# Optimization experiments

Hardware: AMD Instinct MI355X
Metric: run time of the kernel (lower is better)

The kernel has to match this reference:

```python
import jax, jax.numpy as jnp
import numpy as np
from jax import lax

B, C_IN, H, W = 16, 2048, 16, 16
HIDDEN, N_ANC = 512, 9
N_POS, N_NEG = 2048, 2048
TOT = B * N_ANC * H * W  # 36864 = flat conf logits; also rows of reg.view(-1,4)


def _xyxy_to_cxcywh(b):
    x1, y1, x2, y2 = b[..., 0], b[..., 1], b[..., 2], b[..., 3]
    return jnp.stack([(x1 + x2) * 0.5, (y1 + y2) * 0.5, x2 - x1, y2 - y1], axis=-1)


def _cxcywh_to_xyxy(b):
    cx, cy, w, h = b[..., 0], b[..., 1], b[..., 2], b[..., 3]
    return jnp.stack([cx - w * 0.5, cy - h * 0.5, cx + w * 0.5, cy + h * 0.5], axis=-1)


def _rand_boxes(key, n):
    # valid xyxy boxes on the 16x16 feature-map coordinate grid, w,h in [1,4]
    k1, k2 = jax.random.split(key)
    xy = jax.random.uniform(k1, (n, 2), jnp.float32) * 12.0
    wh = 1.0 + jax.random.uniform(k2, (n, 2), jnp.float32) * 3.0
    return jnp.concatenate([xy, xy + wh], axis=-1)


def setup_inputs() -> dict:
    key = jax.random.key(0)
    ks = jax.random.split(key, 10)
    feature_map = jax.random.normal(ks[0], (B, C_IN, H, W), jnp.float32)
    pos_anc_ind = jax.random.randint(ks[1], (N_POS,), 0, TOT)
    neg_anc_ind = jax.random.randint(ks[2], (N_NEG,), 0, TOT)
    pos_anc_coords = _rand_boxes(ks[3], N_POS)
    gt_bboxes_pos = _rand_boxes(ks[4], N_POS)
    s1 = 1.0 / np.sqrt(C_IN * 9)
    W1 = jax.random.uniform(ks[5], (HIDDEN, C_IN, 3, 3), jnp.float32, -s1, s1)
    b1 = jnp.zeros((HIDDEN,), jnp.float32)
    s2 = 1.0 / np.sqrt(HIDDEN)
    Wc = jax.random.uniform(ks[6], (N_ANC, HIDDEN), jnp.float32, -s2, s2)
    bc = jnp.zeros((N_ANC,), jnp.float32)
    Wr = jax.random.uniform(ks[7], (N_ANC * 4, HIDDEN), jnp.float32, -s2, s2)
    br = jnp.zeros((N_ANC * 4,), jnp.float32)
    return {"feature_map": feature_map, "pos_anc_coords": pos_anc_coords,
            "gt_bboxes_pos": gt_bboxes_pos, "W1": W1, "b1": b1, "Wc": Wc,
            "bc": bc, "Wr": Wr, "br": br,
            "pos_anc_ind": pos_anc_ind, "neg_anc_ind": neg_anc_ind}


def generate_proposals(anchors, offsets):
    a = _xyxy_to_cxcywh(anchors)
    p = jnp.stack([a[:, 0] + offsets[:, 0] * a[:, 2],
                   a[:, 1] + offsets[:, 1] * a[:, 3],
                   a[:, 2] * jnp.exp(offsets[:, 2]),
                   a[:, 3] * jnp.exp(offsets[:, 3])], axis=-1)
    return _cxcywh_to_xyxy(p)


def calc_gt_offsets(anc, gt):
    a = _xyxy_to_cxcywh(anc)
    g = _xyxy_to_cxcywh(gt)
    tx = (g[:, 0] - a[:, 0]) / a[:, 2]
    ty = (g[:, 1] - a[:, 1]) / a[:, 3]
    tw = jnp.log(g[:, 2] / a[:, 2])
    th = jnp.log(g[:, 3] / a[:, 3])
    return jnp.stack([tx, ty, tw, th], axis=-1)


def reference(feature_map, pos_anc_coords, gt_bboxes_pos, W1, b1, Wc, bc, Wr, br,
              pos_anc_ind, neg_anc_ind):
    # ProposalModule: conv3x3 -> (dropout=identity in eval) -> relu -> 1x1 heads
    out = lax.conv_general_dilated(feature_map, W1, (1, 1), 'SAME',
                                   dimension_numbers=('NCHW', 'OIHW', 'NCHW'))
    out = jax.nn.relu(out + b1[None, :, None, None])
    conf = jnp.einsum('bchw,oc->bohw', out, Wc) + bc[None, :, None, None]   # [B,9,H,W]
    reg = jnp.einsum('bchw,oc->bohw', out, Wr) + br[None, :, None, None]    # [B,36,H,W]
    # irregular flat gathers, exactly mirroring torch .flatten()/.view(-1,4)
    conf_pos = conf.reshape(-1)[pos_anc_ind]
    conf_neg = conf.reshape(-1)[neg_anc_ind]
    offsets_pos = reg.reshape(-1, 4)[pos_anc_ind]
    proposals = generate_proposals(pos_anc_coords, offsets_pos)
    gt_offsets = calc_gt_offsets(pos_anc_coords, gt_bboxes_pos)
    # BCE-with-logits, targets 1 for pos / 0 for neg, reduction='sum' / B
    cls_loss = (jnp.sum(jax.nn.softplus(-conf_pos)) + jnp.sum(jax.nn.softplus(conf_neg))) / B
    # smooth L1 (beta=1), reduction='sum' / B
    d = offsets_pos - gt_offsets
    ad = jnp.abs(d)
    reg_loss = jnp.sum(jnp.where(ad < 1.0, 0.5 * d * d, ad - 0.5)) / B
    total_rpn_loss = 1.0 * cls_loss + 5.0 * reg_loss  # w_conf=1, w_reg=5
    return total_rpn_loss, proposals
```

## Files before the change

kernel.cpp:

```cpp
#include <hip/hip_runtime.h>
#include <hip/hip_bf16.h>
#include <stdint.h>

#define CIN 2048
#define HID 512
#define NPOS 2048
#define NNEG 2048

#define BM 256
#define BN 256
#define BK 64
#define NS 8
#define A_ELEMS (BM * BK)
#define B_ELEMS (BN * BK)

typedef __attribute__((ext_vector_type(8))) short s16x8;
typedef __attribute__((ext_vector_type(4))) short s16x4;
typedef __attribute__((ext_vector_type(4))) float f32x4;
typedef unsigned short ushort_t;

static __device__ __forceinline__ float bf2f(unsigned short u) {
    union { float f; unsigned int i; } v; v.i = ((unsigned int)u) << 16; return v.f;
}
static __device__ __forceinline__ unsigned short f2bf(float f) {
    union { float f; unsigned int i; } v; v.f = f;
    unsigned int r = v.i + 0x7FFF + ((v.i >> 16) & 1);
    return (unsigned short)(r >> 16);
}

typedef __attribute__((address_space(1))) const void gvoid_t;
typedef __attribute__((address_space(3))) void lvoid_t;
static __device__ __forceinline__ void gload16(const void* g, void* l) {
    __builtin_amdgcn_global_load_lds((gvoid_t*)g, (lvoid_t*)l, 16, 0, 0);
}

__global__ __launch_bounds__(256) void k_prep(const float* __restrict__ F,
                                              const float* __restrict__ W1,
                                              ushort_t* __restrict__ Fp,
                                              ushort_t* __restrict__ Wt2) {
    __shared__ float tile[64][17];
    __shared__ float buf[512 * 9];
    int bid = blockIdx.x;
    int t = threadIdx.x;
    if (bid < 1024) {
        int b = bid >> 6, rem = bid & 63;
        int y = rem >> 2, icq = rem & 3;
        for (int i = 0; i < 8; ++i) {
            int ic0 = icq * 512 + i * 64;
            {
                int ci = t >> 2, xg = t & 3;
                const float4 v = *(const float4*)&F[((size_t)(b * CIN + ic0 + ci) * 16 + y) * 16 + xg * 4];
                tile[ci][xg * 4 + 0] = v.x;
                tile[ci][xg * 4 + 1] = v.y;
                tile[ci][xg * 4 + 2] = v.z;
                tile[ci][xg * 4 + 3] = v.w;
            }
            __syncthreads();
            {
                int x = t >> 4, cig = t & 15;
                s16x4 o;
#pragma unroll
                for (int j = 0; j < 4; ++j) o[j] = (short)f2bf(tile[cig * 4 + j][x]);
                *(s16x4*)&Fp[((size_t)(b * 18 + y + 1) * 18 + (x + 1)) * CIN + ic0 + cig * 4] = o;
            }
            __syncthreads();
        }
    } else if (bid < 1536) {
        int oc = bid - 1024;
        for (int ic0 = 0; ic0 < CIN; ic0 += 512) {
            const float* src = W1 + ((size_t)oc * CIN + ic0) * 9;
            {
                const float4* s4 = (const float4*)src;
                float4* b4 = (float4*)buf;
                for (int i = t; i < 1152; i += 256) b4[i] = s4[i];
            }
            __syncthreads();
            for (int s = t; s < 9 * 64; s += 256) {
                int k = s >> 6, g = s & 63;
                s16x8 v;
#pragma unroll
                for (int j = 0; j < 8; ++j) v[j] = (short)f2bf(buf[(g * 8 + j) * 9 + k]);
                *(s16x8*)&Wt2[((size_t)(k * HID + oc)) * CIN + ic0 + g * 8] = v;
            }
            __syncthreads();
        }
    } else {
        const s16x8 z = {0, 0, 0, 0, 0, 0, 0, 0};
        for (int idx = (bid - 1536) * 256 + t; idx < 16 * 68 * 256; idx += 64 * 256) {
            int seg = idx & 255;
            int cell = (idx >> 8) % 68;
            int b = idx / (68 * 256);
            int Y, X;
            if (cell < 18)      { Y = 0;         X = cell; }
            else if (cell < 36) { Y = 17;        X = cell - 18; }
            else if (cell < 52) { Y = cell - 35; X = 0; }
            else                { Y = cell - 51; X = 17; }
            *(s16x8*)&Fp[((size_t)(b * 18 + Y) * 18 + X) * CIN + seg * 8] = z;
        }
    }
}

__global__ __launch_bounds__(512, 2) void k_gemm(const ushort_t* __restrict__ Fp,
                                                 const ushort_t* __restrict__ Wt2,
                                                 ushort_t* __restrict__ Part,
                                                 int icLen, int nPairs) {
    extern __shared__ ushort_t ldsbuf[];
    ushort_t* As = ldsbuf;
    ushort_t* Bs = ldsbuf + 2 * A_ELEMS;

    int bid = blockIdx.x;
    int rb = bid / nPairs;
    int pair = bid - rb * nPairs;
    int split = pair >> 1, cb = pair & 1;
    int icBase = split * icLen;
    int m0 = rb * BM, oc0 = cb * BN;
    int t = threadIdx.x;
    int wid = t >> 6, lane = t & 63;
    int wr = wid >> 2, wn = wid & 3;
    int hi = lane >> 4, lo = lane & 15;

    f32x4 acc[8][4];
#pragma unroll
    for (int a = 0; a < 8; ++a)
#pragma unroll
        for (int b = 0; b < 4; ++b) acc[a][b] = (f32x4){0.f, 0.f, 0.f, 0.f};

    int Abase[4], Bbase[4];
#pragma unroll
    for (int j = 0; j < 4; ++j) {
        int li = j * 512 + t;
        int row = li >> 3;
        int sg = (li & 7) ^ (row & 7);
        int m = m0 + row;
        int b = m >> 8, y = (m >> 4) & 15, x = m & 15;
        Abase[j] = ((b * 18 + y) * 18 + x) * CIN + sg * 8;
        Bbase[j] = (oc0 + row) * CIN + sg * 8;
    }
    int aidx[8][2], bidx[4][2];
#pragma unroll
    for (int fm = 0; fm < 8; ++fm)
#pragma unroll
        for (int ks = 0; ks < 2; ++ks) {
            int r = wr * 128 + fm * 16 + lo;
            aidx[fm][ks] = r * BK + ((ks * 32 + hi * 8) ^ ((r & 7) << 3));
        }
#pragma unroll
    for (int fn = 0; fn < 4; ++fn)
#pragma unroll
        for (int ks = 0; ks < 2; ++ks) {
            int rB = wn * 64 + fn * 16 + lo;
            bidx[fn][ks] = rB * BK + ((ks * 32 + hi * 8) ^ ((rB & 7) << 3));
        }

    const int nsteps = (icLen / BK) * 9;

#define STAGE(BUF, S)                                                                \
    do {                                                                             \
        int kidx_ = (S) % 9, icc_ = (S) / 9;                                         \
        int ak_ = ((kidx_ / 3) * 18 + (kidx_ - 3 * (kidx_ / 3))) * CIN + icBase + icc_ * BK; \
        int bk_ = kidx_ * HID * CIN + icBase + icc_ * BK;                            \
        ushort_t* dA_ = As + (BUF) * A_ELEMS;                                        \
        ushort_t* dB_ = Bs + (BUF) * B_ELEMS;                                        \
        _Pragma("unroll") for (int j_ = 0; j_ < 4; ++j_) {                           \
            gload16(Fp + Abase[j_] + ak_, dA_ + (size_t)(j_ * 512 + t) * 8);         \
            gload16(Wt2 + Bbase[j_] + bk_, dB_ + (size_t)(j_ * 512 + t) * 8);        \
        }                                                                            \
    } while (0)

    STAGE(0, 0);
    asm volatile("s_waitcnt vmcnt(0)" ::: "memory");
    __builtin_amdgcn_s_barrier();
    __builtin_amdgcn_sched_barrier(0);

    int cur = 0;
#pragma unroll 1
    for (int step = 0; step < nsteps; ++step) {
        const ushort_t* cA = As + cur * A_ELEMS;
        const ushort_t* cB = Bs + cur * B_ELEMS;
        if (step + 1 < nsteps) STAGE(cur ^ 1, step + 1);
        s16x8 af[8][2], bf[4][2];
#pragma unroll
        for (int ks = 0; ks < 2; ++ks) {
#pragma unroll
            for (int fm = 0; fm < 8; ++fm) af[fm][ks] = *(const s16x8*)&cA[aidx[fm][ks]];
#pragma unroll
            for (int fn = 0; fn < 4; ++fn) bf[fn][ks] = *(const s16x8*)&cB[bidx[fn][ks]];
        }
        __builtin_amdgcn_s_setprio(1);
#pragma unroll
        for (int fm = 0; fm < 8; ++fm)
#pragma unroll
            for (int fn = 0; fn < 4; ++fn)
#pragma unroll
                for (int ks = 0; ks < 2; ++ks)
                    acc[fm][fn] = __builtin_amdgcn_mfma_f32_16x16x32_bf16(
                        af[fm][ks], bf[fn][ks], acc[fm][fn], 0, 0, 0);
        __builtin_amdgcn_s_setprio(0);
        if (step + 1 < nsteps) {
            asm volatile("s_waitcnt vmcnt(0)" ::: "memory");
            __builtin_amdgcn_s_barrier();
            __builtin_amdgcn_sched_barrier(0);
        }
        cur ^= 1;
    }
#undef STAGE

#pragma unroll
    for (int fm = 0; fm < 8; ++fm)
#pragma unroll
        for (int fn = 0; fn < 4; ++fn)
#pragma unroll
            for (int r = 0; r < 4; ++r) {
                int gm = m0 + wr * 128 + fm * 16 + hi * 4 + r;
                int gn = oc0 + wn * 64 + fn * 16 + lo;
                Part[((size_t)split * 4096 + gm) * HID + gn] = f2bf(acc[fm][fn][r]);
            }
}

__global__ __launch_bounds__(256) void k_heads(const ushort_t* __restrict__ Part, int ns,
                                               const float* __restrict__ b1,
                                               const float* __restrict__ Wc,
                                               const float* __restrict__ bc,
                                               const float* __restrict__ Wr,
                                               const float* __restrict__ br,
                                               float* __restrict__ conf,
                                               float* __restrict__ reg) {
    extern __shared__ ushort_t hsm[];
    ushort_t* Ah = hsm;
    ushort_t* Wh = hsm + 16 * HID;
    int t = threadIdx.x;
    int wid = t >> 6, lane = t & 63;
    int hi = lane >> 4, lo = lane & 15;
    int row0 = blockIdx.x * 16;

#pragma unroll
    for (int i = 0; i < 4; ++i) {
        int pos = i * 256 + t;
        int r = pos >> 6, sg = pos & 63;
        float s[8];
#pragma unroll
        for (int j = 0; j < 8; ++j) s[j] = 0.f;
        for (int sp = 0; sp < ns; ++sp) {
            s16x8 v = *(const s16x8*)&Part[((size_t)sp * 4096 + row0 + r) * HID + sg * 8];
#pragma unroll
            for (int j = 0; j < 8; ++j) s[j] += bf2f((unsigned short)v[j]);
        }
        s16x8 o;
#pragma unroll
        for (int j = 0; j < 8; ++j) o[j] = (short)f2bf(fmaxf(s[j] + b1[sg * 8 + j], 0.f));
        *(s16x8*)&Ah[r * HID + ((sg ^ (r & 7)) << 3)] = o;
    }
#pragma unroll
    for (int i = 0; i < 12; ++i) {
        int sid = i * 256 + t;
        int o = sid >> 6, sg = sid & 63;
        s16x8 v;
#pragma unroll
        for (int j = 0; j < 8; ++j) {
            float w = 0.f;
            if (o < 9) w = Wc[o * HID + sg * 8 + j];
            else if (o < 45) w = Wr[(size_t)(o - 9) * HID + sg * 8 + j];
            v[j] = (short)f2bf(w);
        }
        *(s16x8*)&Wh[o * HID + ((sg ^ (o & 7)) << 3)] = v;
    }
    __syncthreads();
    if (wid != 0) return;

    f32x4 acc[3];
#pragma unroll
    for (int fn = 0; fn < 3; ++fn) acc[fn] = (f32x4){0.f, 0.f, 0.f, 0.f};
#pragma unroll 1
    for (int kf = 0; kf < 16; ++kf) {
        int rA = lo;
        s16x8 a_ = *(const s16x8*)&Ah[rA * HID + ((kf * 32 + hi * 8) ^ ((rA & 7) << 3))];
#pragma unroll
        for (int fn = 0; fn < 3; ++fn) {
            int rB = fn * 16 + lo;
            s16x8 b_ = *(const s16x8*)&Wh[rB * HID + ((kf * 32 + hi * 8) ^ ((rB & 7) << 3))];
            acc[fn] = __builtin_amdgcn_mfma_f32_16x16x32_bf16(a_, b_, acc[fn], 0, 0, 0);
        }
    }
#pragma unroll
    for (int fn = 0; fn < 3; ++fn)
#pragma unroll
        for (int r = 0; r < 4; ++r) {
            int gm = row0 + hi * 4 + r;
            int o = fn * 16 + lo;
            float v = acc[fn][r];
            if (o < 9) conf[gm * 9 + o] = v + bc[o];
            else if (o < 45) reg[gm * 36 + (o - 9)] = v + br[o - 9];
        }
}

static __device__ __forceinline__ float softplus(float x) {
    return log1pf(expf(-fabsf(x))) + fmaxf(x, 0.f);
}

__global__ __launch_bounds__(1024) void k_loss(const float* __restrict__ conf,
                                               const float* __restrict__ reg,
                                               const int* __restrict__ pos_ind,
                                               const int* __restrict__ neg_ind,
                                               const float* __restrict__ anc,
                                               const float* __restrict__ gt,
                                               float* __restrict__ out) {
    int t = threadIdx.x;
    float cls = 0.f, rloss = 0.f;
    for (int p = t; p < NPOS; p += 1024) {
        int ind = pos_ind[p];
        {
            int b = ind / 2304, r = ind % 2304;
            int c = r >> 8, r2 = r & 255;
            float cv = conf[(b * 256 + r2) * 9 + c];
            cls += softplus(-cv);
        }
        float off[4];
#pragma unroll
        for (int j = 0; j < 4; ++j) {
            int e = 4 * ind + j;
            int b = e / 9216, r = e % 9216;
            int c = r >> 8, r2 = r & 255;
            off[j] = reg[(b * 256 + r2) * 36 + c];
        }
        float ax1 = anc[4 * p], ay1 = anc[4 * p + 1], ax2 = anc[4 * p + 2], ay2 = anc[4 * p + 3];
        float acx = (ax1 + ax2) * 0.5f, acy = (ay1 + ay2) * 0.5f;
        float aw = ax2 - ax1, ah = ay2 - ay1;
        float pcx = acx + off[0] * aw, pcy = acy + off[1] * ah;
        float pw = aw * expf(off[2]), ph = ah * expf(off[3]);
        out[1 + 4 * p + 0] = pcx - pw * 0.5f;
        out[1 + 4 * p + 1] = pcy - ph * 0.5f;
        out[1 + 4 * p + 2] = pcx + pw * 0.5f;
        out[1 + 4 * p + 3] = pcy + ph * 0.5f;
        float gx1 = gt[4 * p], gy1 = gt[4 * p + 1], gx2 = gt[4 * p + 2], gy2 = gt[4 * p + 3];
        float gcx = (gx1 + gx2) * 0.5f, gcy = (gy1 + gy2) * 0.5f;
        float gw = gx2 - gx1, gh = gy2 - gy1;
        float tv[4];
        tv[0] = (gcx - acx) / aw;
        tv[1] = (gcy - acy) / ah;
        tv[2] = logf(gw / aw);
        tv[3] = logf(gh / ah);
#pragma unroll
        for (int j = 0; j < 4; ++j) {
            float d = off[j] - tv[j];
            float ad = fabsf(d);
            rloss += (ad < 1.f) ? 0.5f * d * d : ad - 0.5f;
        }
    }
    for (int q = t; q < NNEG; q += 1024) {
        int ind = neg_ind[q];
        int b = ind / 2304, r = ind % 2304;
        int c = r >> 8, r2 = r & 255;
        float cv = conf[(b * 256 + r2) * 9 + c];
        cls += softplus(cv);
    }
    __shared__ float s1[1024], s2[1024];
    s1[t] = cls;
    s2[t] = rloss;
    __syncthreads();
    for (int s = 512; s > 0; s >>= 1) {
        if (t < s) {
            s1[t] += s1[t + s];
            s2[t] += s2[t + s];
        }
        __syncthreads();
    }
    if (t == 0) out[0] = (s1[0] + 5.f * s2[0]) / 16.f;
}

extern "C" void kernel_launch(void* const* d_in, const int* in_sizes, int n_in,
                              void* d_out, int out_size, void* d_ws, size_t ws_size,
                              hipStream_t stream) {
    const float* F   = (const float*)d_in[0];
    const float* anc = (const float*)d_in[1];
    const float* gt  = (const float*)d_in[2];
    const float* W1  = (const float*)d_in[3];
    const float* b1  = (const float*)d_in[4];
    const float* Wc  = (const float*)d_in[5];
    const float* bc  = (const float*)d_in[6];
    const float* Wr  = (const float*)d_in[7];
    const float* br  = (const float*)d_in[8];
    const int* pos_ind = (const int*)d_in[9];
    const int* neg_ind = (const int*)d_in[10];
    float* out = (float*)d_out;

    char* ws = (char*)d_ws;
    const size_t FP_BYTES   = (size_t)16 * 18 * 18 * CIN * 2;
    const size_t WT_BYTES   = (size_t)9 * HID * CIN * 2;
    const size_t PART_ONE   = (size_t)4096 * HID * 2;
    const size_t CONF_BYTES = (size_t)4096 * 9 * 4;

    int icLen = CIN / NS;

    ushort_t* Fp   = (ushort_t*)ws;
    ushort_t* Wt2  = (ushort_t*)(ws + FP_BYTES);
    ushort_t* Part = (ushort_t*)(ws + FP_BYTES + WT_BYTES);
    float* conf    = (float*)(ws + FP_BYTES + WT_BYTES + (size_t)NS * PART_ONE);
    float* reg     = (float*)(ws + FP_BYTES + WT_BYTES + (size_t)NS * PART_ONE + CONF_BYTES);

    const int GEMM_LDS = 2 * (A_ELEMS + B_ELEMS) * 2;
    hipFuncSetAttribute((const void*)k_gemm, hipFuncAttributeMaxDynamicSharedMemorySize, GEMM_LDS);
    const int HEADS_LDS = (16 + 48) * HID * 2;
    hipFuncSetAttribute((const void*)k_heads, hipFuncAttributeMaxDynamicSharedMemorySize, HEADS_LDS);

    k_prep<<<1600, 256, 0, stream>>>(F, W1, Fp, Wt2);
    k_gemm<<<(4096 / BM) * (HID / BN) * NS, 512, GEMM_LDS, stream>>>(Fp, Wt2, Part, icLen, 2 * NS);
    k_heads<<<256, 256, HEADS_LDS, stream>>>(Part, NS, b1, Wc, bc, Wr, br, conf, reg);
    k_loss<<<1, 1024, 0, stream>>>(conf, reg, pos_ind, neg_ind, anc, gt, out);
}
```

Baseline: 127.5 us.

## Triple-buffer A tiles in conv GEMM and prepack head weights in prep

The conv GEMM now keeps three LDS buffers for the activation tile and two for the weight tile. The activation tile is prefetched two steps ahead and the weight tile one step ahead, with partial vmcnt waits so the in-flight A load is not waited on each step. This aims to hide global-to-LDS latency behind the MFMA work, at the cost of raising LDS use to 160KB per block. Separately, the prep kernel transposes 128 channels per iteration and packs the conf/reg head weights to bf16 once. The heads kernel then loads the packed weights directly with global_load_lds instead of converting them in all 256 blocks.

```diff
diff --git a/kernel.cpp b/kernel.cpp
--- a/kernel.cpp
+++ b/kernel.cpp
@@ -36,19 +36,24 @@
 
 __global__ __launch_bounds__(256) void k_prep(const float* __restrict__ F,
                                               const float* __restrict__ W1,
+                                              const float* __restrict__ Wc,
+                                              const float* __restrict__ Wr,
                                               ushort_t* __restrict__ Fp,
-                                              ushort_t* __restrict__ Wt2) {
-    __shared__ float tile[64][17];
+                                              ushort_t* __restrict__ Wt2,
+                                              ushort_t* __restrict__ Whp) {
+    __shared__ float tile[128][17];
     __shared__ float buf[512 * 9];
     int bid = blockIdx.x;
     int t = threadIdx.x;
     if (bid < 1024) {
         int b = bid >> 6, rem = bid & 63;
         int y = rem >> 2, icq = rem & 3;
-        for (int i = 0; i < 8; ++i) {
-            int ic0 = icq * 512 + i * 64;
-            {
-                int ci = t >> 2, xg = t & 3;
+        for (int it = 0; it < 4; ++it) {
+            int ic0 = icq * 512 + it * 128;
+#pragma unroll
+            for (int i2 = 0; i2 < 2; ++i2) {
+                int idx = i2 * 256 + t;
+                int ci = idx >> 2, xg = idx & 3;
                 const float4 v = *(const float4*)&F[((size_t)(b * CIN + ic0 + ci) * 16 + y) * 16 + xg * 4];
                 tile[ci][xg * 4 + 0] = v.x;
                 tile[ci][xg * 4 + 1] = v.y;
@@ -56,8 +61,10 @@
                 tile[ci][xg * 4 + 3] = v.w;
             }
             __syncthreads();
-            {
-                int x = t >> 4, cig = t & 15;
+#pragma unroll
+            for (int i2 = 0; i2 < 2; ++i2) {
+                int idx = i2 * 256 + t;
+                int x = idx >> 5, cig = idx & 31;
                 s16x4 o;
 #pragma unroll
                 for (int j = 0; j < 4; ++j) o[j] = (short)f2bf(tile[cig * 4 + j][x]);
@@ -84,7 +91,7 @@
             }
             __syncthreads();
         }
-    } else {
+    } else if (bid < 1600) {
         const s16x8 z = {0, 0, 0, 0, 0, 0, 0, 0};
         for (int idx = (bid - 1536) * 256 + t; idx < 16 * 68 * 256; idx += 64 * 256) {
             int seg = idx & 255;
@@ -97,6 +104,21 @@
             else                { Y = cell - 51; X = 17; }
             *(s16x8*)&Fp[((size_t)(b * 18 + Y) * 18 + X) * CIN + seg * 8] = z;
         }
+    } else {
+#pragma unroll
+        for (int i = 0; i < 12; ++i) {
+            int sid = i * 256 + t;
+            int o = sid >> 6, sg = sid & 63;
+            s16x8 v;
+#pragma unroll
+            for (int j = 0; j < 8; ++j) {
+                float w = 0.f;
+                if (o < 9) w = Wc[o * HID + sg * 8 + j];
+                else if (o < 45) w = Wr[(size_t)(o - 9) * HID + sg * 8 + j];
+                v[j] = (short)f2bf(w);
+            }
+            *(s16x8*)&Whp[o * HID + ((sg ^ (o & 7)) << 3)] = v;
+        }
     }
 }
 
@@ -106,7 +128,7 @@
                                                  int icLen, int nPairs) {
     extern __shared__ ushort_t ldsbuf[];
     ushort_t* As = ldsbuf;
-    ushort_t* Bs = ldsbuf + 2 * A_ELEMS;
+    ushort_t* Bs = ldsbuf + 3 * A_ELEMS;
 
     int bid = blockIdx.x;
     int rb = bid / nPairs;
@@ -154,30 +176,33 @@
 
     const int nsteps = (icLen / BK) * 9;
 
-#define STAGE(BUF, S)                                                                \
+#define STAGE_A(BUF, S)                                                              \
     do {                                                                             \
         int kidx_ = (S) % 9, icc_ = (S) / 9;                                         \
         int ak_ = ((kidx_ / 3) * 18 + (kidx_ - 3 * (kidx_ / 3))) * CIN + icBase + icc_ * BK; \
+        ushort_t* dA_ = As + (BUF) * A_ELEMS;                                        \
+        _Pragma("unroll") for (int j_ = 0; j_ < 4; ++j_)                             \
+            gload16(Fp + Abase[j_] + ak_, dA_ + (size_t)(j_ * 512 + t) * 8);         \
+    } while (0)
+#define STAGE_B(BUF, S)                                                              \
+    do {                                                                             \
+        int kidx_ = (S) % 9, icc_ = (S) / 9;                                         \
         int bk_ = kidx_ * HID * CIN + icBase + icc_ * BK;                            \
-        ushort_t* dA_ = As + (BUF) * A_ELEMS;                                        \
         ushort_t* dB_ = Bs + (BUF) * B_ELEMS;                                        \
-        _Pragma("unroll") for (int j_ = 0; j_ < 4; ++j_) {                           \
-            gload16(Fp + Abase[j_] + ak_, dA_ + (size_t)(j_ * 512 + t) * 8);         \
+        _Pragma("unroll") for (int j_ = 0; j_ < 4; ++j_)                             \
             gload16(Wt2 + Bbase[j_] + bk_, dB_ + (size_t)(j_ * 512 + t) * 8);        \
-        }                                                                            \
     } while (0)
 
-    STAGE(0, 0);
-    asm volatile("s_waitcnt vmcnt(0)" ::: "memory");
+    STAGE_A(0, 0); STAGE_B(0, 0); STAGE_A(1, 1);
+    asm volatile("s_waitcnt vmcnt(4)" ::: "memory");
     __builtin_amdgcn_s_barrier();
     __builtin_amdgcn_sched_barrier(0);
 
-    int cur = 0;
 #pragma unroll 1
     for (int step = 0; step < nsteps; ++step) {
-        const ushort_t* cA = As + cur * A_ELEMS;
-        const ushort_t* cB = Bs + cur * B_ELEMS;
-        if (step + 1 < nsteps) STAGE(cur ^ 1, step + 1);
+        const ushort_t* cA = As + (step % 3) * A_ELEMS;
+        const ushort_t* cB = Bs + (step & 1) * B_ELEMS;
+        if (step + 1 < nsteps) STAGE_B((step + 1) & 1, step + 1);
         s16x8 af[8][2], bf[4][2];
 #pragma unroll
         for (int ks = 0; ks < 2; ++ks) {
@@ -186,6 +211,7 @@
 #pragma unroll
             for (int fn = 0; fn < 4; ++fn) bf[fn][ks] = *(const s16x8*)&cB[bidx[fn][ks]];
         }
+        if (step + 2 < nsteps) STAGE_A((step + 2) % 3, step + 2);
         __builtin_amdgcn_s_setprio(1);
 #pragma unroll
         for (int fm = 0; fm < 8; ++fm)
@@ -196,14 +222,18 @@
                     acc[fm][fn] = __builtin_amdgcn_mfma_f32_16x16x32_bf16(
                         af[fm][ks], bf[fn][ks], acc[fm][fn], 0, 0, 0);
         __builtin_amdgcn_s_setprio(0);
-        if (step + 1 < nsteps) {
+        if (step + 2 < nsteps) {
+            asm volatile("s_waitcnt vmcnt(4)" ::: "memory");
+            __builtin_amdgcn_s_barrier();
+            __builtin_amdgcn_sched_barrier(0);
+        } else if (step + 1 < nsteps) {
             asm volatile("s_waitcnt vmcnt(0)" ::: "memory");
             __builtin_amdgcn_s_barrier();
             __builtin_amdgcn_sched_barrier(0);
         }
-        cur ^= 1;
-    }
-#undef STAGE
+    }
+#undef STAGE_A
+#undef STAGE_B
 
 #pragma unroll
     for (int fm = 0; fm < 8; ++fm)
@@ -218,10 +248,9 @@
 }
 
 __global__ __launch_bounds__(256) void k_heads(const ushort_t* __restrict__ Part, int ns,
+                                               const ushort_t* __restrict__ Whp,
                                                const float* __restrict__ b1,
-                                               const float* __restrict__ Wc,
                                                const float* __restrict__ bc,
-                                               const float* __restrict__ Wr,
                                                const float* __restrict__ br,
                                                float* __restrict__ conf,
                                                float* __restrict__ reg) {
@@ -234,6 +263,10 @@
     int row0 = blockIdx.x * 16;
 
 #pragma unroll
+    for (int i = 0; i < 12; ++i)
+        gload16(Whp + (size_t)(i * 256 + t) * 8, Wh + (size_t)(i * 256 + t) * 8);
+
+#pragma unroll
     for (int i = 0; i < 4; ++i) {
         int pos = i * 256 + t;
         int r = pos >> 6, sg = pos & 63;
@@ -249,20 +282,6 @@
 #pragma unroll
         for (int j = 0; j < 8; ++j) o[j] = (short)f2bf(fmaxf(s[j] + b1[sg * 8 + j], 0.f));
         *(s16x8*)&Ah[r * HID + ((sg ^ (r & 7)) << 3)] = o;
-    }
-#pragma unroll
-    for (int i = 0; i < 12; ++i) {
-        int sid = i * 256 + t;
-        int o = sid >> 6, sg = sid & 63;
-        s16x8 v;
-#pragma unroll
-        for (int j = 0; j < 8; ++j) {
-            float w = 0.f;
-            if (o < 9) w = Wc[o * HID + sg * 8 + j];
-            else if (o < 45) w = Wr[(size_t)(o - 9) * HID + sg * 8 + j];
-            v[j] = (short)f2bf(w);
-        }
-        *(s16x8*)&Wh[o * HID + ((sg ^ (o & 7)) << 3)] = v;
     }
     __syncthreads();
     if (wid != 0) return;
@@ -388,6 +407,7 @@
     const size_t WT_BYTES   = (size_t)9 * HID * CIN * 2;
     const size_t PART_ONE   = (size_t)4096 * HID * 2;
     const size_t CONF_BYTES = (size_t)4096 * 9 * 4;
+    const size_t REG_BYTES  = (size_t)4096 * 36 * 4;
 
     int icLen = CIN / NS;
 
@@ -396,14 +416,15 @@
     ushort_t* Part = (ushort_t*)(ws + FP_BYTES + WT_BYTES);
     float* conf    = (float*)(ws + FP_BYTES + WT_BYTES + (size_t)NS * PART_ONE);
     float* reg     = (float*)(ws + FP_BYTES + WT_BYTES + (size_t)NS * PART_ONE + CONF_BYTES);
-
-    const int GEMM_LDS = 2 * (A_ELEMS + B_ELEMS) * 2;
+    ushort_t* Whp  = (ushort_t*)(ws + FP_BYTES + WT_BYTES + (size_t)NS * PART_ONE + CONF_BYTES + REG_BYTES);
+
+    const int GEMM_LDS = (3 * A_ELEMS + 2 * B_ELEMS) * 2;
     hipFuncSetAttribute((const void*)k_gemm, hipFuncAttributeMaxDynamicSharedMemorySize, GEMM_LDS);
     const int HEADS_LDS = (16 + 48) * HID * 2;
     hipFuncSetAttribute((const void*)k_heads, hipFuncAttributeMaxDynamicSharedMemorySize, HEADS_LDS);
 
-    k_prep<<<1600, 256, 0, stream>>>(F, W1, Fp, Wt2);
+    k_prep<<<1601, 256, 0, stream>>>(F, W1, Wc, Wr, Fp, Wt2, Whp);
     k_gemm<<<(4096 / BM) * (HID / BN) * NS, 512, GEMM_LDS, stream>>>(Fp, Wt2, Part, icLen, 2 * NS);
-    k_heads<<<256, 256, HEADS_LDS, stream>>>(Part, NS, b1, Wc, bc, Wr, br, conf, reg);
+    k_heads<<<256, 256, HEADS_LDS, stream>>>(Part, NS, Whp, b1, bc, br, conf, reg);
     k_loss<<<1, 1024, 0, stream>>>(conf, reg, pos_ind, neg_ind, anc, gt, out);
 }
```

Result: no change. 125.4 us, median of 2 (-1.6%).
